# Performance work log

Measured on AMD Instinct MI355X. Metric: run time of the kernel, lower is better.

The kernel has to match this reference:

```python
import jax, jax.numpy as jnp
import numpy as np

D_MODEL = 1024
DIM_FF = 4096
N_EXPERTS = 8
TOPK = 2
N_TOKENS = 8192


def setup_inputs() -> dict:
    key = jax.random.key(0)
    ks = jax.random.split(key, 8)
    s_in = 1.0 / np.sqrt(D_MODEL)
    s_ff = 1.0 / np.sqrt(DIM_FF)
    x = jax.random.normal(ks[0], (N_TOKENS, D_MODEL), dtype=jnp.float32)
    Wg = jax.random.uniform(ks[1], (D_MODEL, N_EXPERTS), minval=-s_in, maxval=s_in, dtype=jnp.float32)
    bg = jax.random.uniform(ks[2], (N_EXPERTS,), minval=-s_in, maxval=s_in, dtype=jnp.float32)
    W1 = jax.random.uniform(ks[3], (N_EXPERTS, D_MODEL, DIM_FF), minval=-s_in, maxval=s_in, dtype=jnp.float32)
    b1 = jax.random.uniform(ks[4], (N_EXPERTS, DIM_FF), minval=-s_in, maxval=s_in, dtype=jnp.float32)
    W2 = jax.random.uniform(ks[5], (N_EXPERTS, DIM_FF, D_MODEL), minval=-s_ff, maxval=s_ff, dtype=jnp.float32)
    b2 = jax.random.uniform(ks[6], (N_EXPERTS, D_MODEL), minval=-s_ff, maxval=s_ff, dtype=jnp.float32)
    return {"x": x, "Wg": Wg, "bg": bg, "W1": W1, "b1": b1, "W2": W2, "b2": b2}


def reference(x, Wg, bg, W1, b1, W2, b2):
    # Gate: softmax over experts
    w = jax.nn.softmax(x @ Wg + bg, axis=-1)  # [N, E]
    # Sparse gating: keep top-k, renormalize (matches torch scatter mask)
    _, idx = jax.lax.top_k(w, TOPK)  # [N, K]
    n = w.shape[0]
    mask = jnp.zeros_like(w).at[jnp.arange(n)[:, None], idx].set(1.0)
    w = w * mask
    w = w / (jnp.sum(w, axis=-1, keepdims=True) + 1e-9)
    # Dense per-expert FFN (exact GELU, as torch nn.GELU default)
    h = jax.nn.gelu(jnp.einsum('nd,edf->enf', x, W1) + b1[:, None, :], approximate=False)  # [E,N,F]
    y = jnp.einsum('enf,efd->end', h, W2) + b2[:, None, :]  # [E,N,D]
    out = jnp.einsum('ne,end->nd', w, y)  # weighted combine
    return out
```

## Files before the change

### kernel.cpp

```cpp
#include <hip/hip_runtime.h>
#include <cstdint>

typedef unsigned short u16;
typedef unsigned int u32;

#define N_TOKENS 8192
#define D_MODEL 1024
#define DIM_FF 4096
#define N_EXPERTS 8
#define MAX_SLOTS (N_TOKENS * 2)

typedef __bf16 bf16x8 __attribute__((ext_vector_type(8)));
typedef float f32x4 __attribute__((ext_vector_type(4)));

__device__ __forceinline__ u16 f2bf(float f) {
  u32 u = __float_as_uint(f);
  u32 r = (u + 0x7FFFu + ((u >> 16) & 1u)) >> 16;
  return (u16)r;
}
__device__ __forceinline__ u16 bfc(float f) {
  __bf16 b = (__bf16)f;
  return __builtin_bit_cast(u16, b);
}

__device__ __forceinline__ void gl2lds16(const void* g, void* l) {
  __builtin_amdgcn_global_load_lds(
      (__attribute__((address_space(1))) void*)(g),
      (__attribute__((address_space(3))) void*)(l), 16, 0, 0);
}

__global__ __launch_bounds__(256) void gate_kernel(
    const float* __restrict__ x, const float* __restrict__ Wg,
    const float* __restrict__ bg, int* __restrict__ eidx,
    float* __restrict__ ew, u16* __restrict__ xb) {
  int tok = (int)((blockIdx.x * 256 + threadIdx.x) >> 6);
  int lane = threadIdx.x & 63;
  const float* xr = x + (size_t)tok * D_MODEL;
  u16* xbr = xb + (size_t)tok * D_MODEL;
  float acc[8] = {0.f, 0.f, 0.f, 0.f, 0.f, 0.f, 0.f, 0.f};
#pragma unroll
  for (int j = 0; j < 8; ++j) {
    int d = 2 * lane + 128 * j;
    float2 xv = *(const float2*)(xr + d);
    float4 wa0 = *(const float4*)(Wg + d * 8);
    float4 wb0 = *(const float4*)(Wg + d * 8 + 4);
    float4 wa1 = *(const float4*)(Wg + d * 8 + 8);
    float4 wb1 = *(const float4*)(Wg + d * 8 + 12);
    acc[0] += xv.x * wa0.x + xv.y * wa1.x;
    acc[1] += xv.x * wa0.y + xv.y * wa1.y;
    acc[2] += xv.x * wa0.z + xv.y * wa1.z;
    acc[3] += xv.x * wa0.w + xv.y * wa1.w;
    acc[4] += xv.x * wb0.x + xv.y * wb1.x;
    acc[5] += xv.x * wb0.y + xv.y * wb1.y;
    acc[6] += xv.x * wb0.z + xv.y * wb1.z;
    acc[7] += xv.x * wb0.w + xv.y * wb1.w;
    u32 pk = (u32)f2bf(xv.x) | ((u32)f2bf(xv.y) << 16);
    *(u32*)(xbr + d) = pk;
  }
#pragma unroll
  for (int off = 32; off > 0; off >>= 1) {
#pragma unroll
    for (int e = 0; e < 8; ++e) acc[e] += __shfl_xor(acc[e], off, 64);
  }
  if (lane == 0) {
    float p[8], m = -1e30f;
#pragma unroll
    for (int e = 0; e < 8; ++e) { p[e] = acc[e] + bg[e]; m = fmaxf(m, p[e]); }
    float s = 0.f;
#pragma unroll
    for (int e = 0; e < 8; ++e) { p[e] = __expf(p[e] - m); s += p[e]; }
#pragma unroll
    for (int e = 0; e < 8; ++e) p[e] /= s;
    int i0 = 0;
#pragma unroll
    for (int e = 1; e < 8; ++e) if (p[e] > p[i0]) i0 = e;
    int i1 = (i0 == 0) ? 1 : 0;
#pragma unroll
    for (int e = 0; e < 8; ++e) if (e != i0 && p[e] > p[i1]) i1 = e;
    float denom = p[i0] + p[i1] + 1e-9f;
    eidx[2 * tok] = i0; eidx[2 * tok + 1] = i1;
    ew[2 * tok] = p[i0] / denom; ew[2 * tok + 1] = p[i1] / denom;
  }
}

__global__ __launch_bounds__(256) void count_kernel(const int* __restrict__ eidx,
                                                    int* __restrict__ counts) {
  __shared__ int lc[16];
  int tid = threadIdx.x;
  if (tid < 16) lc[tid] = 0;
  __syncthreads();
  int t = blockIdx.x * 256 + tid;
  atomicAdd(&lc[2 * eidx[2 * t]], 1);
  atomicAdd(&lc[2 * eidx[2 * t + 1] + 1], 1);
  __syncthreads();
  if (tid < 16) atomicAdd(&counts[tid], lc[tid]);
}

__global__ __launch_bounds__(256) void fill_kernel(
    const int* __restrict__ eidx, const float* __restrict__ ew,
    const int* __restrict__ counts, int* __restrict__ fill,
    int* __restrict__ rowtok, float* __restrict__ rowwt) {
  __shared__ int lc[16];
  __shared__ int lbase[16];
  __shared__ int loff[16];
  int tid = threadIdx.x;
  if (tid < 16) lc[tid] = 0;
  __syncthreads();
  int t = blockIdx.x * 256 + tid;
  int e0 = eidx[2 * t], e1 = eidx[2 * t + 1];
  int p0 = atomicAdd(&lc[2 * e0], 1);
  int p1 = atomicAdd(&lc[2 * e1 + 1], 1);
  __syncthreads();
  if (tid < 16) lbase[tid] = atomicAdd(&fill[tid], lc[tid]);
  if (tid == 64) {
    int o = 0;
    for (int g = 0; g < 16; ++g) { loff[g] = o; o += counts[g]; }
  }
  __syncthreads();
  int pos0 = loff[2 * e0] + lbase[2 * e0] + p0;
  int pos1 = loff[2 * e1 + 1] + lbase[2 * e1 + 1] + p1;
  rowtok[pos0] = t; rowwt[pos0] = ew[2 * t];
  rowtok[pos1] = t; rowwt[pos1] = ew[2 * t + 1];
}

__global__ __launch_bounds__(256) void transpose_cvt(const float* __restrict__ in,
                                                     u16* __restrict__ out, int R, int C) {
  int e = blockIdx.z;
  const float* ip = in + (size_t)e * R * C;
  u16* op = out + (size_t)e * R * C;
  int c0 = blockIdx.x * 64, r0 = blockIdx.y * 64;
  __shared__ __align__(16) u16 t[64 * 68];
  int tid = threadIdx.x;
  int c4 = (tid & 15) * 4;
#pragma unroll
  for (int p = 0; p < 4; ++p) {
    int r = (tid >> 4) + 16 * p;
    float4 v = *(const float4*)(ip + (size_t)(r0 + r) * C + c0 + c4);
    uint2 pk;
    pk.x = (u32)bfc(v.x) | ((u32)bfc(v.y) << 16);
    pk.y = (u32)bfc(v.z) | ((u32)bfc(v.w) << 16);
    *(uint2*)&t[r * 68 + c4] = pk;
  }
  __syncthreads();
  int pair = tid >> 3;
  int r8 = (tid & 7) * 8;
  int c = 2 * pair;
  u32 u[8];
#pragma unroll
  for (int j = 0; j < 8; ++j) u[j] = *(const u32*)&t[(r8 + j) * 68 + c];
  uint4 lo, hi;
  lo.x = (u[0] & 0xffffu) | (u[1] << 16);
  lo.y = (u[2] & 0xffffu) | (u[3] << 16);
  lo.z = (u[4] & 0xffffu) | (u[5] << 16);
  lo.w = (u[6] & 0xffffu) | (u[7] << 16);
  hi.x = (u[0] >> 16) | (u[1] & 0xffff0000u);
  hi.y = (u[2] >> 16) | (u[3] & 0xffff0000u);
  hi.z = (u[4] >> 16) | (u[5] & 0xffff0000u);
  hi.w = (u[6] >> 16) | (u[7] & 0xffff0000u);
  *(uint4*)(op + (size_t)(c0 + c) * R + r0 + r8) = lo;
  *(uint4*)(op + (size_t)(c0 + c + 1) * R + r0 + r8) = hi;
}

__global__ __launch_bounds__(256) void fc1_kernel(
    const u16* __restrict__ xb, const u16* __restrict__ w1t,
    const float* __restrict__ b1, const int* __restrict__ rowtok,
    const int* __restrict__ counts, u16* __restrict__ H) {
  const int b = blockIdx.x;
  const int e = b & 7;
  const int lin = b >> 3;
  const int rt = lin & 63;
  const int ct = lin >> 6;
  int base = 0;
#pragma unroll
  for (int g = 0; g < 16; ++g) base += (g < 2 * e) ? counts[g] : 0;
  const int count = counts[2 * e] + counts[2 * e + 1];
  if (rt * 128 >= count) return;

  __shared__ __align__(16) __bf16 As[128 * 32];
  __shared__ __align__(16) __bf16 Bs[128 * 32];

  const int tid = threadIdx.x;
  const int lane = tid & 63;
  const int wave = tid >> 6;

  const int ra = tid >> 2;
  const int lastslot = base + count - 1;
  int s0 = base + rt * 128 + ra;       if (s0 > lastslot) s0 = lastslot;
  int s1 = base + rt * 128 + ra + 64;  if (s1 > lastslot) s1 = lastslot;
  const size_t koff = (size_t)(tid & 3) * 8;
  const u16* ga0 = xb + (size_t)rowtok[s0] * D_MODEL + koff;
  const u16* ga1 = xb + (size_t)rowtok[s1] * D_MODEL + koff;
  const u16* gb0 = w1t + (size_t)e * DIM_FF * D_MODEL + (size_t)(ct * 128 + ra) * D_MODEL + koff;
  const u16* gb1 = gb0 + (size_t)64 * D_MODEL;

  __bf16* lA0 = As + tid * 8;
  __bf16* lA1 = As + (tid + 256) * 8;
  __bf16* lB0 = Bs + tid * 8;
  __bf16* lB1 = Bs + (tid + 256) * 8;

  const int wm = (wave & 1) * 64;
  const int wn = (wave >> 1) * 64;
  const int quad = lane >> 4;
  const int lc = lane & 15;
  const __bf16* Ap = As + (wm + lc) * 32 + quad * 8;
  const __bf16* Bp = Bs + (wn + lc) * 32 + quad * 8;

  f32x4 acc[4][4];
#pragma unroll
  for (int i = 0; i < 4; ++i)
#pragma unroll
    for (int j = 0; j < 4; ++j) acc[i][j] = (f32x4)0.0f;

  for (int kt = 0; kt < D_MODEL / 32; ++kt) {
    gl2lds16(ga0 + kt * 32, lA0);
    gl2lds16(ga1 + kt * 32, lA1);
    gl2lds16(gb0 + kt * 32, lB0);
    gl2lds16(gb1 + kt * 32, lB1);
    __syncthreads();
    bf16x8 af[4], bfr[4];
#pragma unroll
    for (int mi = 0; mi < 4; ++mi) af[mi] = *(const bf16x8*)(Ap + mi * 16 * 32);
#pragma unroll
    for (int ni = 0; ni < 4; ++ni) bfr[ni] = *(const bf16x8*)(Bp + ni * 16 * 32);
#pragma unroll
    for (int mi = 0; mi < 4; ++mi)
#pragma unroll
      for (int ni = 0; ni < 4; ++ni)
        acc[mi][ni] = __builtin_amdgcn_mfma_f32_16x16x32_bf16(af[mi], bfr[ni], acc[mi][ni], 0, 0, 0);
    __syncthreads();
  }

  float bias[4];
#pragma unroll
  for (int ni = 0; ni < 4; ++ni) bias[ni] = b1[e * DIM_FF + ct * 128 + wn + ni * 16 + lc];
#pragma unroll
  for (int mi = 0; mi < 4; ++mi) {
#pragma unroll
    for (int r = 0; r < 4; ++r) {
      int m = wm + mi * 16 + quad * 4 + r;
      int grow = rt * 128 + m;
      if (grow < count) {
        size_t rowbase = (size_t)(base + grow) * DIM_FF + ct * 128 + wn;
#pragma unroll
        for (int ni = 0; ni < 4; ++ni) {
          float v = acc[mi][ni][r] + bias[ni];
          float t3 = v * (1.0f + 0.044715f * v * v);
          float u = __builtin_amdgcn_exp2f(fminf(2.302208f * t3, 80.0f));
          float h = v * u * __builtin_amdgcn_rcpf(u + 1.0f);
          H[rowbase + ni * 16 + lc] = f2bf(h);
        }
      }
    }
  }
}

__global__ __launch_bounds__(256) void fc2_kernel(
    const u16* __restrict__ H, const u16* __restrict__ w2t,
    const float* __restrict__ b2, const int* __restrict__ rowtok,
    const float* __restrict__ rowwt, const int* __restrict__ counts,
    float* __restrict__ out, int kpass) {
  const int b = blockIdx.x;
  const int e = b & 7;
  const int lin = b >> 3;
  const int rt = lin & 63;
  const int ct = lin >> 6;
  int base = 0;
#pragma unroll
  for (int g = 0; g < 16; ++g) base += (g < 2 * e + kpass) ? counts[g] : 0;
  const int cnt = counts[2 * e + kpass];
  if (rt * 128 >= cnt) return;

  __shared__ __align__(16) __bf16 As[128 * 32];
  __shared__ __align__(16) __bf16 Bs[128 * 32];

  const int tid = threadIdx.x;
  const int lane = tid & 63;
  const int wave = tid >> 6;

  const int ra = tid >> 2;
  const size_t koff = (size_t)(tid & 3) * 8;
  const u16* ga0 = H + (size_t)(base + rt * 128 + ra) * DIM_FF + koff;
  const u16* ga1 = ga0 + (size_t)64 * DIM_FF;
  const u16* gb0 = w2t + (size_t)e * D_MODEL * DIM_FF + (size_t)(ct * 128 + ra) * DIM_FF + koff;
  const u16* gb1 = gb0 + (size_t)64 * DIM_FF;

  __bf16* lA0 = As + tid * 8;
  __bf16* lA1 = As + (tid + 256) * 8;
  __bf16* lB0 = Bs + tid * 8;
  __bf16* lB1 = Bs + (tid + 256) * 8;

  const int wm = (wave & 1) * 64;
  const int wn = (wave >> 1) * 64;
  const int quad = lane >> 4;
  const int lc = lane & 15;
  const __bf16* Ap = As + (wm + lc) * 32 + quad * 8;
  const __bf16* Bp = Bs + (wn + lc) * 32 + quad * 8;

  f32x4 acc[4][4];
#pragma unroll
  for (int i = 0; i < 4; ++i)
#pragma unroll
    for (int j = 0; j < 4; ++j) acc[i][j] = (f32x4)0.0f;

  for (int kt = 0; kt < DIM_FF / 32; ++kt) {
    gl2lds16(ga0 + kt * 32, lA0);
    gl2lds16(ga1 + kt * 32, lA1);
    gl2lds16(gb0 + kt * 32, lB0);
    gl2lds16(gb1 + kt * 32, lB1);
    __syncthreads();
    bf16x8 af[4], bfr[4];
#pragma unroll
    for (int mi = 0; mi < 4; ++mi) af[mi] = *(const bf16x8*)(Ap + mi * 16 * 32);
#pragma unroll
    for (int ni = 0; ni < 4; ++ni) bfr[ni] = *(const bf16x8*)(Bp + ni * 16 * 32);
#pragma unroll
    for (int mi = 0; mi < 4; ++mi)
#pragma unroll
      for (int ni = 0; ni < 4; ++ni)
        acc[mi][ni] = __builtin_amdgcn_mfma_f32_16x16x32_bf16(af[mi], bfr[ni], acc[mi][ni], 0, 0, 0);
    __syncthreads();
  }

  float bias[4];
#pragma unroll
  for (int ni = 0; ni < 4; ++ni) bias[ni] = b2[e * D_MODEL + ct * 128 + wn + ni * 16 + lc];

#pragma unroll
  for (int mi = 0; mi < 4; ++mi) {
#pragma unroll
    for (int r = 0; r < 4; ++r) {
      int m = wm + mi * 16 + quad * 4 + r;
      int grow = rt * 128 + m;
      if (grow < cnt) {
        int slot = base + grow;
        float wt = rowwt[slot];
        float* orow = out + (size_t)rowtok[slot] * D_MODEL + ct * 128 + wn;
        if (kpass == 0) {
#pragma unroll
          for (int ni = 0; ni < 4; ++ni)
            orow[ni * 16 + lc] = wt * (acc[mi][ni][r] + bias[ni]);
        } else {
#pragma unroll
          for (int ni = 0; ni < 4; ++ni)
            orow[ni * 16 + lc] += wt * (acc[mi][ni][r] + bias[ni]);
        }
      }
    }
  }
}

extern "C" void kernel_launch(void* const* d_in, const int* in_sizes, int n_in,
                              void* d_out, int out_size, void* d_ws, size_t ws_size,
                              hipStream_t stream) {
  (void)in_sizes; (void)n_in; (void)ws_size; (void)out_size;
  const float* x  = (const float*)d_in[0];
  const float* Wg = (const float*)d_in[1];
  const float* bg = (const float*)d_in[2];
  const float* W1 = (const float*)d_in[3];
  const float* b1 = (const float*)d_in[4];
  const float* W2 = (const float*)d_in[5];
  const float* b2 = (const float*)d_in[6];
  float* out = (float*)d_out;

  char* ws = (char*)d_ws;
  size_t off = 0;
  int*   counts  = (int*)(ws + 0);
  int*   fill    = (int*)(ws + 128);
  off = 4096;
  int*   eidx    = (int*)(ws + off); off += 65536;
  float* ew      = (float*)(ws + off); off += 65536;
  int*   rowtok  = (int*)(ws + off); off += 65536;
  float* rowwt   = (float*)(ws + off); off += 65536;
  u16*   xb      = (u16*)(ws + off); off += (size_t)N_TOKENS * D_MODEL * 2;
  u16*   w1t     = (u16*)(ws + off);
  u16*   w2t     = w1t;
  off += (size_t)N_EXPERTS * DIM_FF * D_MODEL * 2;
  u16*   H       = (u16*)(ws + off);
  off += (size_t)(MAX_SLOTS + 128) * DIM_FF * 2;

  hipMemsetAsync(ws, 0, 4096, stream);

  gate_kernel<<<N_TOKENS / 4, 256, 0, stream>>>(x, Wg, bg, eidx, ew, xb);
  count_kernel<<<N_TOKENS / 256, 256, 0, stream>>>(eidx, counts);
  fill_kernel<<<N_TOKENS / 256, 256, 0, stream>>>(eidx, ew, counts, fill, rowtok, rowwt);
  transpose_cvt<<<dim3(DIM_FF / 64, D_MODEL / 64, N_EXPERTS), 256, 0, stream>>>(W1, w1t, D_MODEL, DIM_FF);
  fc1_kernel<<<N_EXPERTS * (DIM_FF / 128) * 64, 256, 0, stream>>>(xb, w1t, b1, rowtok, counts, H);
  transpose_cvt<<<dim3(D_MODEL / 64, DIM_FF / 64, N_EXPERTS), 256, 0, stream>>>(W2, w2t, DIM_FF, D_MODEL);
  fc2_kernel<<<N_EXPERTS * (D_MODEL / 128) * 64, 256, 0, stream>>>(H, w2t, b2, rowtok, rowwt, counts, out, 0);
  fc2_kernel<<<N_EXPERTS * (D_MODEL / 128) * 64, 256, 0, stream>>>(H, w2t, b2, rowtok, rowwt, counts, out, 1);
}
```

Before: 776.6 us.

## Double-buffer LDS tiles in FFN GEMMs and merge fc2 passes with atomics

Both expert GEMM kernels now use two LDS buffers and issue the next k-tile's global-to-LDS loads before computing the current tile. The goal is to overlap memory latency with MFMA work. The two fc2 launches (top-1 and top-2 slots) are merged into one launch over all slots of an expert, which accumulates into a zeroed output with float atomics. This removes a launch and the partially empty grids, at the cost of atomic traffic, a memset, and doubled shared memory that may lower occupancy.

```diff
diff --git a/kernel.cpp b/kernel.cpp
--- a/kernel.cpp
+++ b/kernel.cpp
@@ -176,8 +176,8 @@
   const int count = counts[2 * e] + counts[2 * e + 1];
   if (rt * 128 >= count) return;
 
-  __shared__ __align__(16) __bf16 As[128 * 32];
-  __shared__ __align__(16) __bf16 Bs[128 * 32];
+  __shared__ __align__(16) __bf16 As[2][128 * 32];
+  __shared__ __align__(16) __bf16 Bs[2][128 * 32];
 
   const int tid = threadIdx.x;
   const int lane = tid & 63;
@@ -193,17 +193,10 @@
   const u16* gb0 = w1t + (size_t)e * DIM_FF * D_MODEL + (size_t)(ct * 128 + ra) * D_MODEL + koff;
   const u16* gb1 = gb0 + (size_t)64 * D_MODEL;
 
-  __bf16* lA0 = As + tid * 8;
-  __bf16* lA1 = As + (tid + 256) * 8;
-  __bf16* lB0 = Bs + tid * 8;
-  __bf16* lB1 = Bs + (tid + 256) * 8;
-
   const int wm = (wave & 1) * 64;
   const int wn = (wave >> 1) * 64;
   const int quad = lane >> 4;
   const int lc = lane & 15;
-  const __bf16* Ap = As + (wm + lc) * 32 + quad * 8;
-  const __bf16* Bp = Bs + (wn + lc) * 32 + quad * 8;
 
   f32x4 acc[4][4];
 #pragma unroll
@@ -211,12 +204,23 @@
 #pragma unroll
     for (int j = 0; j < 4; ++j) acc[i][j] = (f32x4)0.0f;
 
-  for (int kt = 0; kt < D_MODEL / 32; ++kt) {
-    gl2lds16(ga0 + kt * 32, lA0);
-    gl2lds16(ga1 + kt * 32, lA1);
-    gl2lds16(gb0 + kt * 32, lB0);
-    gl2lds16(gb1 + kt * 32, lB1);
-    __syncthreads();
+  const int NT = D_MODEL / 32;
+  gl2lds16(ga0, As[0] + tid * 8);
+  gl2lds16(ga1, As[0] + (tid + 256) * 8);
+  gl2lds16(gb0, Bs[0] + tid * 8);
+  gl2lds16(gb1, Bs[0] + (tid + 256) * 8);
+  __syncthreads();
+  int cur = 0;
+  for (int kt = 0; kt < NT; ++kt) {
+    if (kt + 1 < NT) {
+      const int nb = cur ^ 1;
+      gl2lds16(ga0 + (kt + 1) * 32, As[nb] + tid * 8);
+      gl2lds16(ga1 + (kt + 1) * 32, As[nb] + (tid + 256) * 8);
+      gl2lds16(gb0 + (kt + 1) * 32, Bs[nb] + tid * 8);
+      gl2lds16(gb1 + (kt + 1) * 32, Bs[nb] + (tid + 256) * 8);
+    }
+    const __bf16* Ap = As[cur] + (wm + lc) * 32 + quad * 8;
+    const __bf16* Bp = Bs[cur] + (wn + lc) * 32 + quad * 8;
     bf16x8 af[4], bfr[4];
 #pragma unroll
     for (int mi = 0; mi < 4; ++mi) af[mi] = *(const bf16x8*)(Ap + mi * 16 * 32);
@@ -228,6 +232,7 @@
       for (int ni = 0; ni < 4; ++ni)
         acc[mi][ni] = __builtin_amdgcn_mfma_f32_16x16x32_bf16(af[mi], bfr[ni], acc[mi][ni], 0, 0, 0);
     __syncthreads();
+    cur ^= 1;
   }
 
   float bias[4];
@@ -258,7 +263,7 @@
     const u16* __restrict__ H, const u16* __restrict__ w2t,
     const float* __restrict__ b2, const int* __restrict__ rowtok,
     const float* __restrict__ rowwt, const int* __restrict__ counts,
-    float* __restrict__ out, int kpass) {
+    float* __restrict__ out) {
   const int b = blockIdx.x;
   const int e = b & 7;
   const int lin = b >> 3;
@@ -266,12 +271,12 @@
   const int ct = lin >> 6;
   int base = 0;
 #pragma unroll
-  for (int g = 0; g < 16; ++g) base += (g < 2 * e + kpass) ? counts[g] : 0;
-  const int cnt = counts[2 * e + kpass];
+  for (int g = 0; g < 16; ++g) base += (g < 2 * e) ? counts[g] : 0;
+  const int cnt = counts[2 * e] + counts[2 * e + 1];
   if (rt * 128 >= cnt) return;
 
-  __shared__ __align__(16) __bf16 As[128 * 32];
-  __shared__ __align__(16) __bf16 Bs[128 * 32];
+  __shared__ __align__(16) __bf16 As[2][128 * 32];
+  __shared__ __align__(16) __bf16 Bs[2][128 * 32];
 
   const int tid = threadIdx.x;
   const int lane = tid & 63;
@@ -284,17 +289,10 @@
   const u16* gb0 = w2t + (size_t)e * D_MODEL * DIM_FF + (size_t)(ct * 128 + ra) * DIM_FF + koff;
   const u16* gb1 = gb0 + (size_t)64 * DIM_FF;
 
-  __bf16* lA0 = As + tid * 8;
-  __bf16* lA1 = As + (tid + 256) * 8;
-  __bf16* lB0 = Bs + tid * 8;
-  __bf16* lB1 = Bs + (tid + 256) * 8;
-
   const int wm = (wave & 1) * 64;
   const int wn = (wave >> 1) * 64;
   const int quad = lane >> 4;
   const int lc = lane & 15;
-  const __bf16* Ap = As + (wm + lc) * 32 + quad * 8;
-  const __bf16* Bp = Bs + (wn + lc) * 32 + quad * 8;
 
   f32x4 acc[4][4];
 #pragma unroll
@@ -302,12 +300,23 @@
 #pragma unroll
     for (int j = 0; j < 4; ++j) acc[i][j] = (f32x4)0.0f;
 
-  for (int kt = 0; kt < DIM_FF / 32; ++kt) {
-    gl2lds16(ga0 + kt * 32, lA0);
-    gl2lds16(ga1 + kt * 32, lA1);
-    gl2lds16(gb0 + kt * 32, lB0);
-    gl2lds16(gb1 + kt * 32, lB1);
-    __syncthreads();
+  const int NT = DIM_FF / 32;
+  gl2lds16(ga0, As[0] + tid * 8);
+  gl2lds16(ga1, As[0] + (tid + 256) * 8);
+  gl2lds16(gb0, Bs[0] + tid * 8);
+  gl2lds16(gb1, Bs[0] + (tid + 256) * 8);
+  __syncthreads();
+  int cur = 0;
+  for (int kt = 0; kt < NT; ++kt) {
+    if (kt + 1 < NT) {
+      const int nb = cur ^ 1;
+      gl2lds16(ga0 + (kt + 1) * 32, As[nb] + tid * 8);
+      gl2lds16(ga1 + (kt + 1) * 32, As[nb] + (tid + 256) * 8);
+      gl2lds16(gb0 + (kt + 1) * 32, Bs[nb] + tid * 8);
+      gl2lds16(gb1 + (kt + 1) * 32, Bs[nb] + (tid + 256) * 8);
+    }
+    const __bf16* Ap = As[cur] + (wm + lc) * 32 + quad * 8;
+    const __bf16* Bp = Bs[cur] + (wn + lc) * 32 + quad * 8;
     bf16x8 af[4], bfr[4];
 #pragma unroll
     for (int mi = 0; mi < 4; ++mi) af[mi] = *(const bf16x8*)(Ap + mi * 16 * 32);
@@ -319,6 +328,7 @@
       for (int ni = 0; ni < 4; ++ni)
         acc[mi][ni] = __builtin_amdgcn_mfma_f32_16x16x32_bf16(af[mi], bfr[ni], acc[mi][ni], 0, 0, 0);
     __syncthreads();
+    cur ^= 1;
   }
 
   float bias[4];
@@ -335,15 +345,9 @@
         int slot = base + grow;
         float wt = rowwt[slot];
         float* orow = out + (size_t)rowtok[slot] * D_MODEL + ct * 128 + wn;
-        if (kpass == 0) {
-#pragma unroll
-          for (int ni = 0; ni < 4; ++ni)
-            orow[ni * 16 + lc] = wt * (acc[mi][ni][r] + bias[ni]);
-        } else {
-#pragma unroll
-          for (int ni = 0; ni < 4; ++ni)
-            orow[ni * 16 + lc] += wt * (acc[mi][ni][r] + bias[ni]);
-        }
+#pragma unroll
+        for (int ni = 0; ni < 4; ++ni)
+          unsafeAtomicAdd(orow + ni * 16 + lc, wt * (acc[mi][ni][r] + bias[ni]));
       }
     }
   }
@@ -379,6 +383,7 @@
   off += (size_t)(MAX_SLOTS + 128) * DIM_FF * 2;
 
   hipMemsetAsync(ws, 0, 4096, stream);
+  hipMemsetAsync(out, 0, (size_t)N_TOKENS * D_MODEL * sizeof(float), stream);
 
   gate_kernel<<<N_TOKENS / 4, 256, 0, stream>>>(x, Wg, bg, eidx, ew, xb);
   count_kernel<<<N_TOKENS / 256, 256, 0, stream>>>(eidx, counts);
@@ -386,6 +391,5 @@
   transpose_cvt<<<dim3(DIM_FF / 64, D_MODEL / 64, N_EXPERTS), 256, 0, stream>>>(W1, w1t, D_MODEL, DIM_FF);
   fc1_kernel<<<N_EXPERTS * (DIM_FF / 128) * 64, 256, 0, stream>>>(xb, w1t, b1, rowtok, counts, H);
   transpose_cvt<<<dim3(D_MODEL / 64, DIM_FF / 64, N_EXPERTS), 256, 0, stream>>>(W2, w2t, DIM_FF, D_MODEL);
-  fc2_kernel<<<N_EXPERTS * (D_MODEL / 128) * 64, 256, 0, stream>>>(H, w2t, b2, rowtok, rowwt, counts, out, 0);
-  fc2_kernel<<<N_EXPERTS * (D_MODEL / 128) * 64, 256, 0, stream>>>(H, w2t, b2, rowtok, rowwt, counts, out, 1);
-}
+  fc2_kernel<<<N_EXPERTS * (D_MODEL / 128) * 64, 256, 0, stream>>>(H, w2t, b2, rowtok, rowwt, counts, out);
+}
```

Measured after the change: 843.1 us. 1.09x slower.

## Double K tile to 64 with XOR-swizzled LDS layout in FC1/FC2 GEMMs

Applied to the files above, without the earlier changes.

Both expert GEMM kernels now stage a 64-wide K slice per iteration instead of 32, which halves the number of barrier pairs per output tile. The LDS rows become 128 bytes, so an XOR swizzle on the 16-byte chunk index is applied on both the global-to-LDS writes and the fragment reads to avoid bank conflicts. Each iteration now issues two MFMA groups. LDS use doubles to 32 KB per block, which may limit occupancy.

```diff
diff --git a/kernel.cpp b/kernel.cpp
--- a/kernel.cpp
+++ b/kernel.cpp
@@ -161,6 +161,7 @@
   *(uint4*)(op + (size_t)(c0 + c + 1) * R + r0 + r8) = hi;
 }
 
+
 __global__ __launch_bounds__(256) void fc1_kernel(
     const u16* __restrict__ xb, const u16* __restrict__ w1t,
     const float* __restrict__ b1, const int* __restrict__ rowtok,
@@ -176,34 +177,36 @@
   const int count = counts[2 * e] + counts[2 * e + 1];
   if (rt * 128 >= count) return;
 
-  __shared__ __align__(16) __bf16 As[128 * 32];
-  __shared__ __align__(16) __bf16 Bs[128 * 32];
+  __shared__ __align__(16) __bf16 As[128 * 64];
+  __shared__ __align__(16) __bf16 Bs[128 * 64];
 
   const int tid = threadIdx.x;
   const int lane = tid & 63;
   const int wave = tid >> 6;
 
-  const int ra = tid >> 2;
+  const int srow = tid >> 3;
+  const int schunk = tid & 7;
+  const int sx = ((schunk ^ (srow & 7)) * 8);
   const int lastslot = base + count - 1;
-  int s0 = base + rt * 128 + ra;       if (s0 > lastslot) s0 = lastslot;
-  int s1 = base + rt * 128 + ra + 64;  if (s1 > lastslot) s1 = lastslot;
-  const size_t koff = (size_t)(tid & 3) * 8;
-  const u16* ga0 = xb + (size_t)rowtok[s0] * D_MODEL + koff;
-  const u16* ga1 = xb + (size_t)rowtok[s1] * D_MODEL + koff;
-  const u16* gb0 = w1t + (size_t)e * DIM_FF * D_MODEL + (size_t)(ct * 128 + ra) * D_MODEL + koff;
-  const u16* gb1 = gb0 + (size_t)64 * D_MODEL;
-
-  __bf16* lA0 = As + tid * 8;
-  __bf16* lA1 = As + (tid + 256) * 8;
-  __bf16* lB0 = Bs + tid * 8;
-  __bf16* lB1 = Bs + (tid + 256) * 8;
+  const u16* gA[4];
+  const u16* gB[4];
+  const u16* wb = w1t + (size_t)e * DIM_FF * D_MODEL + (size_t)(ct * 128) * D_MODEL;
+#pragma unroll
+  for (int p = 0; p < 4; ++p) {
+    int s = base + rt * 128 + srow + 32 * p;
+    if (s > lastslot) s = lastslot;
+    gA[p] = xb + (size_t)rowtok[s] * D_MODEL + sx;
+    gB[p] = wb + (size_t)(srow + 32 * p) * D_MODEL + sx;
+  }
 
   const int wm = (wave & 1) * 64;
   const int wn = (wave >> 1) * 64;
   const int quad = lane >> 4;
   const int lc = lane & 15;
-  const __bf16* Ap = As + (wm + lc) * 32 + quad * 8;
-  const __bf16* Bp = Bs + (wn + lc) * 32 + quad * 8;
+  const int cx0 = ((0 + quad) ^ (lc & 7)) * 8;
+  const int cx1 = ((4 + quad) ^ (lc & 7)) * 8;
+  const __bf16* Ap = As + (wm + lc) * 64;
+  const __bf16* Bp = Bs + (wn + lc) * 64;
 
   f32x4 acc[4][4];
 #pragma unroll
@@ -211,17 +214,27 @@
 #pragma unroll
     for (int j = 0; j < 4; ++j) acc[i][j] = (f32x4)0.0f;
 
-  for (int kt = 0; kt < D_MODEL / 32; ++kt) {
-    gl2lds16(ga0 + kt * 32, lA0);
-    gl2lds16(ga1 + kt * 32, lA1);
-    gl2lds16(gb0 + kt * 32, lB0);
-    gl2lds16(gb1 + kt * 32, lB1);
+  for (int kt = 0; kt < D_MODEL / 64; ++kt) {
+#pragma unroll
+    for (int p = 0; p < 4; ++p) {
+      gl2lds16(gA[p] + (size_t)kt * 64, (char*)As + p * 4096 + tid * 16);
+      gl2lds16(gB[p] + (size_t)kt * 64, (char*)Bs + p * 4096 + tid * 16);
+    }
     __syncthreads();
     bf16x8 af[4], bfr[4];
 #pragma unroll
-    for (int mi = 0; mi < 4; ++mi) af[mi] = *(const bf16x8*)(Ap + mi * 16 * 32);
-#pragma unroll
-    for (int ni = 0; ni < 4; ++ni) bfr[ni] = *(const bf16x8*)(Bp + ni * 16 * 32);
+    for (int mi = 0; mi < 4; ++mi) af[mi] = *(const bf16x8*)(Ap + mi * 16 * 64 + cx0);
+#pragma unroll
+    for (int ni = 0; ni < 4; ++ni) bfr[ni] = *(const bf16x8*)(Bp + ni * 16 * 64 + cx0);
+#pragma unroll
+    for (int mi = 0; mi < 4; ++mi)
+#pragma unroll
+      for (int ni = 0; ni < 4; ++ni)
+        acc[mi][ni] = __builtin_amdgcn_mfma_f32_16x16x32_bf16(af[mi], bfr[ni], acc[mi][ni], 0, 0, 0);
+#pragma unroll
+    for (int mi = 0; mi < 4; ++mi) af[mi] = *(const bf16x8*)(Ap + mi * 16 * 64 + cx1);
+#pragma unroll
+    for (int ni = 0; ni < 4; ++ni) bfr[ni] = *(const bf16x8*)(Bp + ni * 16 * 64 + cx1);
 #pragma unroll
     for (int mi = 0; mi < 4; ++mi)
 #pragma unroll
@@ -270,31 +283,34 @@
   const int cnt = counts[2 * e + kpass];
   if (rt * 128 >= cnt) return;
 
-  __shared__ __align__(16) __bf16 As[128 * 32];
-  __shared__ __align__(16) __bf16 Bs[128 * 32];
+  __shared__ __align__(16) __bf16 As[128 * 64];
+  __shared__ __align__(16) __bf16 Bs[128 * 64];
 
   const int tid = threadIdx.x;
   const int lane = tid & 63;
   const int wave = tid >> 6;
 
-  const int ra = tid >> 2;
-  const size_t koff = (size_t)(tid & 3) * 8;
-  const u16* ga0 = H + (size_t)(base + rt * 128 + ra) * DIM_FF + koff;
-  const u16* ga1 = ga0 + (size_t)64 * DIM_FF;
-  const u16* gb0 = w2t + (size_t)e * D_MODEL * DIM_FF + (size_t)(ct * 128 + ra) * DIM_FF + koff;
-  const u16* gb1 = gb0 + (size_t)64 * DIM_FF;
-
-  __bf16* lA0 = As + tid * 8;
-  __bf16* lA1 = As + (tid + 256) * 8;
-  __bf16* lB0 = Bs + tid * 8;
-  __bf16* lB1 = Bs + (tid + 256) * 8;
+  const int srow = tid >> 3;
+  const int schunk = tid & 7;
+  const int sx = ((schunk ^ (srow & 7)) * 8);
+  const u16* gA[4];
+  const u16* gB[4];
+  const u16* hb = H + (size_t)(base + rt * 128) * DIM_FF;
+  const u16* wb = w2t + (size_t)e * D_MODEL * DIM_FF + (size_t)(ct * 128) * DIM_FF;
+#pragma unroll
+  for (int p = 0; p < 4; ++p) {
+    gA[p] = hb + (size_t)(srow + 32 * p) * DIM_FF + sx;
+    gB[p] = wb + (size_t)(srow + 32 * p) * DIM_FF + sx;
+  }
 
   const int wm = (wave & 1) * 64;
   const int wn = (wave >> 1) * 64;
   const int quad = lane >> 4;
   const int lc = lane & 15;
-  const __bf16* Ap = As + (wm + lc) * 32 + quad * 8;
-  const __bf16* Bp = Bs + (wn + lc) * 32 + quad * 8;
+  const int cx0 = ((0 + quad) ^ (lc & 7)) * 8;
+  const int cx1 = ((4 + quad) ^ (lc & 7)) * 8;
+  const __bf16* Ap = As + (wm + lc) * 64;
+  const __bf16* Bp = Bs + (wn + lc) * 64;
 
   f32x4 acc[4][4];
 #pragma unroll
@@ -302,17 +318,27 @@
 #pragma unroll
     for (int j = 0; j < 4; ++j) acc[i][j] = (f32x4)0.0f;
 
-  for (int kt = 0; kt < DIM_FF / 32; ++kt) {
-    gl2lds16(ga0 + kt * 32, lA0);
-    gl2lds16(ga1 + kt * 32, lA1);
-    gl2lds16(gb0 + kt * 32, lB0);
-    gl2lds16(gb1 + kt * 32, lB1);
+  for (int kt = 0; kt < DIM_FF / 64; ++kt) {
+#pragma unroll
+    for (int p = 0; p < 4; ++p) {
+      gl2lds16(gA[p] + (size_t)kt * 64, (char*)As + p * 4096 + tid * 16);
+      gl2lds16(gB[p] + (size_t)kt * 64, (char*)Bs + p * 4096 + tid * 16);
+    }
     __syncthreads();
     bf16x8 af[4], bfr[4];
 #pragma unroll
-    for (int mi = 0; mi < 4; ++mi) af[mi] = *(const bf16x8*)(Ap + mi * 16 * 32);
-#pragma unroll
-    for (int ni = 0; ni < 4; ++ni) bfr[ni] = *(const bf16x8*)(Bp + ni * 16 * 32);
+    for (int mi = 0; mi < 4; ++mi) af[mi] = *(const bf16x8*)(Ap + mi * 16 * 64 + cx0);
+#pragma unroll
+    for (int ni = 0; ni < 4; ++ni) bfr[ni] = *(const bf16x8*)(Bp + ni * 16 * 64 + cx0);
+#pragma unroll
+    for (int mi = 0; mi < 4; ++mi)
+#pragma unroll
+      for (int ni = 0; ni < 4; ++ni)
+        acc[mi][ni] = __builtin_amdgcn_mfma_f32_16x16x32_bf16(af[mi], bfr[ni], acc[mi][ni], 0, 0, 0);
+#pragma unroll
+    for (int mi = 0; mi < 4; ++mi) af[mi] = *(const bf16x8*)(Ap + mi * 16 * 64 + cx1);
+#pragma unroll
+    for (int ni = 0; ni < 4; ++ni) bfr[ni] = *(const bf16x8*)(Bp + ni * 16 * 64 + cx1);
 #pragma unroll
     for (int mi = 0; mi < 4; ++mi)
 #pragma unroll
```

Result: slower. 814.9 us (+4.9%).
